# Optimization experiments

Hardware: AMD Instinct MI355X
Metric: run time of the kernel (lower is better)

Reference implementation:

```python
import jax, jax.numpy as jnp
import numpy as np

D = 512        # model dim
NH = 8         # heads
NL = 4         # layers
MSL = 2048     # max_seq_len for relative positional bias
ITEM_V, CATE_V, SEG_V = 100000, 1000, 2
EPS = 1e-5


def layer_norm(x, w, b):
    mu = jnp.mean(x, axis=-1, keepdims=True)
    var = jnp.mean((x - mu) ** 2, axis=-1, keepdims=True)
    return (x - mu) * jax.lax.rsqrt(var + EPS) * w + b


def setup_inputs() -> dict:
    key = jax.random.key(0)
    ks = jax.random.split(key, 16)
    B, L = 8, 1023
    inp = {
        'historical_item_ids': jax.random.randint(ks[0], (B, L), 0, ITEM_V, dtype=jnp.int32),
        'historical_cate_ids': jax.random.randint(ks[1], (B, L), 0, CATE_V, dtype=jnp.int32),
        'historical_len': jax.random.randint(ks[2], (B,), 0, L, dtype=jnp.int32),
        'target_item_id': jax.random.randint(ks[3], (B,), 0, ITEM_V, dtype=jnp.int32),
        'target_cate_id': jax.random.randint(ks[4], (B,), 0, CATE_V, dtype=jnp.int32),
        # embeddings (init std 0.02 like _init_weights)
        'item_emb': 0.02 * jax.random.normal(ks[5], (ITEM_V, D), jnp.float32),
        'cate_emb': 0.02 * jax.random.normal(ks[6], (CATE_V, D), jnp.float32),
        'seg_emb': 0.02 * jax.random.normal(ks[7], (SEG_V, D), jnp.float32),
        # per-layer stacked params
        'W1': 0.02 * jax.random.normal(ks[8], (NL, D, 4 * D), jnp.float32),
        'b1': jnp.zeros((NL, 4 * D), jnp.float32),
        'W2': 0.02 * jax.random.normal(ks[9], (NL, D, D), jnp.float32),
        'b2': jnp.zeros((NL, D), jnp.float32),
        'ln1_w': jnp.ones((NL, D), jnp.float32), 'ln1_b': jnp.zeros((NL, D), jnp.float32),
        'ln2_w': jnp.ones((NL, D), jnp.float32), 'ln2_b': jnp.zeros((NL, D), jnp.float32),
        'pos_w': 0.02 * jax.random.normal(ks[10], (NL, 2 * MSL - 1), jnp.float32),
        'lnf_w': jnp.ones((D,), jnp.float32), 'lnf_b': jnp.zeros((D,), jnp.float32),
    }
    return inp


def _forward(historical_item_ids, historical_cate_ids, historical_len,
             target_item_id, target_cate_id,
             item_emb, cate_emb, seg_emb, W1, b1, W2, b2,
             ln1_w, ln1_b, ln2_w, ln2_b, pos_w, lnf_w, lnf_b):
    B = historical_item_ids.shape[0]
    ar = jnp.arange(B)
    pad = jnp.zeros((B, 1), historical_item_ids.dtype)
    ids = jnp.concatenate([historical_item_ids, pad], axis=1).at[ar, historical_len].set(target_item_id)
    cids = jnp.concatenate([historical_cate_ids, pad], axis=1).at[ar, historical_len].set(target_cate_id)
    S = ids.shape[1]
    seg = jnp.zeros_like(ids).at[ar, historical_len].set(1)

    h = item_emb[ids] + cate_emb[cids] + seg_emb[seg]  # [B,S,D]

    # relative position bias indices: bias[i,j] = pos_w[MSL-1 + j - i]
    rel_idx = MSL - 1 + jnp.arange(S)[None, :] - jnp.arange(S)[:, None]  # [S,S]
    causal = jnp.tril(jnp.ones((S, S), h.dtype))  # multiplicative mask (mask >= 0)

    for l in range(NL):
        z = jax.nn.silu(h @ W1[l] + b1[l])  # [B,S,4D]
        u, q, k, v = jnp.split(z, 4, axis=-1)
        resh = lambda t: t.reshape(B, S, NH, D // NH).transpose(0, 2, 1, 3)  # [B,H,S,hd]
        u, q, k, v = resh(u), resh(q), resh(k), resh(v)
        bias = pos_w[l][rel_idx]  # [S,S]
        att = jax.nn.silu(jnp.einsum('bhsd,bhtd->bhst', q, k) + bias) * causal
        y = jnp.einsum('bhst,bhtd->bhsd', att, v) * u
        y = y.transpose(0, 2, 1, 3).reshape(B, S, D)
        y = layer_norm(y, ln1_w[l], ln1_b[l])
        y = y @ W2[l] + b2[l]
        h = layer_norm(y + h, ln2_w[l], ln2_b[l])  # dropout p=0 (eval)

    return layer_norm(h, lnf_w, lnf_b)


def reference(historical_item_ids, historical_cate_ids, historical_len,
              target_item_id, target_cate_id,
              item_emb, cate_emb, seg_emb, W1, b1, W2, b2,
              ln1_w, ln1_b, ln2_w, ln2_b, pos_w, lnf_w, lnf_b):
    return _forward(historical_item_ids, historical_cate_ids, historical_len,
                    target_item_id, target_cate_id,
                    item_emb, cate_emb, seg_emb, W1, b1, W2, b2,
                    ln1_w, ln1_b, ln2_w, ln2_b, pos_w, lnf_w, lnf_b)
```

## Files before the change

### kernel.cpp

```cpp
#include <hip/hip_runtime.h>
#include <cstddef>


#define D_MODEL 512
#define S_LEN 1024
#define NHEADS 8

typedef __bf16 bf16x8 __attribute__((ext_vector_type(8)));
typedef float f32x4 __attribute__((ext_vector_type(4)));
typedef unsigned short us4 __attribute__((ext_vector_type(4)));
typedef unsigned short us8 __attribute__((ext_vector_type(8)));

__device__ __forceinline__ float silu_f(float x) {
  return x / (1.f + __expf(-x));
}
__device__ __forceinline__ unsigned short f2bf(float f) {
  unsigned int u = __float_as_uint(f);
  u += 0x7FFF + ((u >> 16) & 1);
  return (unsigned short)(u >> 16);
}
__device__ __forceinline__ float bf2f(unsigned short s) {
  return __uint_as_float(((unsigned int)s) << 16);
}
__device__ __forceinline__ void gll16(const void* g, void* l) {
  __builtin_amdgcn_global_load_lds(
      (const __attribute__((address_space(1))) unsigned int*)g,
      (__attribute__((address_space(3))) unsigned int*)l, 16, 0, 0);
}

__global__ __launch_bounds__(256) void embed_kernel(
    const int* __restrict__ hist_i, const int* __restrict__ hist_c,
    const int* __restrict__ hlen, const int* __restrict__ tgt_i,
    const int* __restrict__ tgt_c, const float* __restrict__ item_emb,
    const float* __restrict__ cate_emb, const float* __restrict__ seg_emb,
    float* __restrict__ h32, unsigned short* __restrict__ hbf) {
  int bs = blockIdx.x;
  int b = bs >> 10, s = bs & 1023;
  int l = hlen[b];
  int id, cid, sg;
  if (s == l)       { id = tgt_i[b]; cid = tgt_c[b]; sg = 1; }
  else if (s < 1023){ id = hist_i[b * 1023 + s]; cid = hist_c[b * 1023 + s]; sg = 0; }
  else              { id = 0; cid = 0; sg = 0; }
  const float* ie = item_emb + (size_t)id * D_MODEL;
  const float* ce = cate_emb + (size_t)cid * D_MODEL;
  const float* se = seg_emb + (size_t)sg * D_MODEL;
  float* hr = h32 + (size_t)bs * D_MODEL;
  unsigned short* hb = hbf + (size_t)bs * D_MODEL;
  for (int d = threadIdx.x; d < D_MODEL; d += 256) {
    float v = ie[d] + ce[d] + se[d];
    hr[d] = v;
    hb[d] = f2bf(v);
  }
}

__global__ __launch_bounds__(256) void transpose_kernel(
    const float* __restrict__ W, unsigned short* __restrict__ Wt,
    int K, int N) {
  const int l = blockIdx.z;
  W += (size_t)l * K * N;
  Wt += (size_t)l * K * N;
  const int n0 = blockIdx.x * 64, k0 = blockIdx.y * 64;
  __shared__ float T[64][65];
  const int tid = threadIdx.x;
  const int rr = tid >> 4, cc = (tid & 15) * 4;
#pragma unroll
  for (int p = 0; p < 4; p++) {
    const int r = rr + p * 16;
    const float4 v = *reinterpret_cast<const float4*>(&W[(size_t)(k0 + r) * N + n0 + cc]);
    T[r][cc] = v.x; T[r][cc + 1] = v.y; T[r][cc + 2] = v.z; T[r][cc + 3] = v.w;
  }
  __syncthreads();
#pragma unroll
  for (int p = 0; p < 4; p++) {
    const int r = rr + p * 16;
    us4 o = { f2bf(T[cc + 0][r]), f2bf(T[cc + 1][r]),
              f2bf(T[cc + 2][r]), f2bf(T[cc + 3][r]) };
    *reinterpret_cast<us4*>(&Wt[(size_t)(n0 + r) * K + k0 + cc]) = o;
  }
}

template <int TM, int TN, int SWZ, int EPI_SILU, typename OutT>
__global__ __launch_bounds__(256) void mfma_gemm(
    const unsigned short* __restrict__ A, const unsigned short* __restrict__ Bt,
    const float* __restrict__ bias, OutT* __restrict__ C,
    int M, int N, int K) {
  constexpr int MI = TM / 32, NI = TN / 32;
  __shared__ unsigned short As[2][TM * 64];
  __shared__ unsigned short Bs[2][TN * 64];
  const int tid = threadIdx.x;
  const int w = tid >> 6, lane = tid & 63, lm = lane & 15, quad = lane >> 4;
  const int wm = w & 1, wn = w >> 1;
  int m0, n0;
  if (SWZ) {
    const int id = blockIdx.x;
    const int xcd = id & 7, j = id >> 3;
    const int mPerX = (M / TM) >> 3;
    m0 = (xcd * mPerX + (j % mPerX)) * TM;
    n0 = (j / mPerX) * TN;
  } else {
    m0 = blockIdx.y * TM;
    n0 = blockIdx.x * TN;
  }

  f32x4 acc[MI][NI] = {};

  auto stage = [&](int buf, int k0) {
#pragma unroll
    for (int p = 0; p < TM / 32; p++) {
      const int g = p * 256 + tid;
      const int r = g >> 3;
      const int lc = (g & 7) ^ (r & 7);
      gll16(A + (size_t)(m0 + r) * K + k0 + lc * 8, &As[buf][g * 8]);
    }
#pragma unroll
    for (int p = 0; p < TN / 32; p++) {
      const int g = p * 256 + tid;
      const int r = g >> 3;
      const int lc = (g & 7) ^ (r & 7);
      gll16(Bt + (size_t)(n0 + r) * K + k0 + lc * 8, &Bs[buf][g * 8]);
    }
  };

  stage(0, 0);
  __syncthreads();
  int cur = 0;

  for (int k0 = 0; k0 < K; k0 += 64) {
    if (k0 + 64 < K) stage(cur ^ 1, k0 + 64);
#pragma unroll
    for (int ki = 0; ki < 2; ki++) {
      bf16x8 af[MI], bfr[NI];
#pragma unroll
      for (int mi = 0; mi < MI; mi++) {
        const int r = wm * (TM / 2) + mi * 16 + lm;
        const int p = (ki * 4 + quad) ^ (lm & 7);
        af[mi] = *reinterpret_cast<const bf16x8*>(&As[cur][r * 64 + p * 8]);
      }
#pragma unroll
      for (int ni = 0; ni < NI; ni++) {
        const int r = wn * (TN / 2) + ni * 16 + lm;
        const int p = (ki * 4 + quad) ^ (lm & 7);
        bfr[ni] = *reinterpret_cast<const bf16x8*>(&Bs[cur][r * 64 + p * 8]);
      }
#pragma unroll
      for (int mi = 0; mi < MI; mi++)
#pragma unroll
        for (int ni = 0; ni < NI; ni++)
          acc[mi][ni] = __builtin_amdgcn_mfma_f32_16x16x32_bf16(
              af[mi], bfr[ni], acc[mi][ni], 0, 0, 0);
    }
    __syncthreads();
    cur ^= 1;
  }

#pragma unroll
  for (int ni = 0; ni < NI; ni++) {
    const int n = n0 + wn * (TN / 2) + ni * 16 + lm;
    const float bv = bias[n];
#pragma unroll
    for (int mi = 0; mi < MI; mi++) {
      const int mbase = m0 + wm * (TM / 2) + mi * 16 + quad * 4;
#pragma unroll
      for (int reg = 0; reg < 4; reg++) {
        float v = acc[mi][ni][reg] + bv;
        if (EPI_SILU) v = silu_f(v);
        if constexpr (sizeof(OutT) == 2)
          C[(size_t)(mbase + reg) * N + n] = f2bf(v);
        else
          C[(size_t)(mbase + reg) * N + n] = v;
      }
    }
  }
}

#define LDR 72
__global__ __launch_bounds__(256) void attn_kernel(
    const unsigned short* __restrict__ z, const float* __restrict__ posw,
    unsigned short* __restrict__ y) {
  const int hh = blockIdx.y, b = blockIdx.z;
  __shared__ alignas(16) unsigned short Ks[2 * 64 * LDR];
  __shared__ alignas(16) unsigned short Vt[2 * 64 * LDR];
  __shared__ alignas(16) unsigned short Ps[64 * LDR];
  __shared__ float bias_s[2][128];
  const unsigned short* zb = z + (size_t)b * S_LEN * 2048;
  const int tid = threadIdx.x;
  const int w = tid >> 6, lane = tid & 63, lm = lane & 15, quad = lane >> 4;

  const int kr0r = tid >> 3, kr0c = (tid & 7) * 8;
  const int kr1r = (256 + tid) >> 3, kr1c = (tid & 7) * 8;
  const int vt = (tid >> 4) * 4, vd = (tid & 15) * 4;
  const int vtb = vt >> 3, vti = vt & 7;

#pragma unroll
  for (int phase = 0; phase < 2; phase++) {
    const int qt = phase == 0 ? (int)blockIdx.x : 15 - (int)blockIdx.x;
    const int s0 = qt * 64;
    const int srow = s0 + w * 16 + lm;

    const bf16x8 qb0 = *reinterpret_cast<const bf16x8*>(
        zb + (size_t)srow * 2048 + 512 + hh * 64 + quad * 8);
    const bf16x8 qb1 = *reinterpret_cast<const bf16x8*>(
        zb + (size_t)srow * 2048 + 512 + hh * 64 + 32 + quad * 8);

    f32x4 O[4] = {};

    us8 kr0, kr1;
    us4 vr0, vr1, vr2, vr3;
    float br = 0.f;

    auto load_stage = [&](int kt) {
      const int t0 = kt * 64;
      kr0 = *reinterpret_cast<const us8*>(
          zb + (size_t)(t0 + kr0r) * 2048 + 1024 + hh * 64 + kr0c);
      kr1 = *reinterpret_cast<const us8*>(
          zb + (size_t)(t0 + kr1r) * 2048 + 1024 + hh * 64 + kr1c);
      vr0 = *reinterpret_cast<const us4*>(
          zb + (size_t)(t0 + vt + 0) * 2048 + 1536 + hh * 64 + vd);
      vr1 = *reinterpret_cast<const us4*>(
          zb + (size_t)(t0 + vt + 1) * 2048 + 1536 + hh * 64 + vd);
      vr2 = *reinterpret_cast<const us4*>(
          zb + (size_t)(t0 + vt + 2) * 2048 + 1536 + hh * 64 + vd);
      vr3 = *reinterpret_cast<const us4*>(
          zb + (size_t)(t0 + vt + 3) * 2048 + 1536 + hh * 64 + vd);
      if (tid < 128) br = posw[2047 + t0 - s0 - 63 + tid];
    };

    auto write_stage = [&](int cur) {
      unsigned short* KsC = Ks + cur * (64 * LDR);
      unsigned short* VtC = Vt + cur * (64 * LDR);
      *reinterpret_cast<us8*>(&KsC[kr0r * LDR + kr0c]) = kr0;
      *reinterpret_cast<us8*>(&KsC[kr1r * LDR + kr1c]) = kr1;
      unsigned short c[4][4];
      c[0][0] = vr0.x; c[0][1] = vr0.y; c[0][2] = vr0.z; c[0][3] = vr0.w;
      c[1][0] = vr1.x; c[1][1] = vr1.y; c[1][2] = vr1.z; c[1][3] = vr1.w;
      c[2][0] = vr2.x; c[2][1] = vr2.y; c[2][2] = vr2.z; c[2][3] = vr2.w;
      c[3][0] = vr3.x; c[3][1] = vr3.y; c[3][2] = vr3.z; c[3][3] = vr3.w;
#pragma unroll
      for (int j = 0; j < 4; j++) {
        const int dd = vd + j;
        us4 o = { c[0][j], c[1][j], c[2][j], c[3][j] };
        *reinterpret_cast<us4*>(&VtC[dd * LDR + ((vtb ^ (dd & 7)) << 3) + vti]) = o;
      }
      if (tid < 128) bias_s[cur][tid] = br;
    };

    load_stage(0);
    __syncthreads();

    for (int kt = 0; kt <= qt; kt++) {
      const int cur = kt & 1;
      write_stage(cur);
      __syncthreads();
      if (kt < qt) load_stage(kt + 1);

      const unsigned short* KsC = Ks + cur * (64 * LDR);
      const unsigned short* VtC = Vt + cur * (64 * LDR);
      const int t0 = kt * 64;

#pragma unroll
      for (int tt = 0; tt < 4; tt++) {
        const bf16x8 ka0 = *reinterpret_cast<const bf16x8*>(
            &KsC[(tt * 16 + lm) * LDR + quad * 8]);
        const bf16x8 ka1 = *reinterpret_cast<const bf16x8*>(
            &KsC[(tt * 16 + lm) * LDR + 32 + quad * 8]);
        f32x4 st = {};
        __builtin_amdgcn_s_setprio(1);
        st = __builtin_amdgcn_mfma_f32_16x16x32_bf16(ka0, qb0, st, 0, 0, 0);
        st = __builtin_amdgcn_mfma_f32_16x16x32_bf16(ka1, qb1, st, 0, 0, 0);
        __builtin_amdgcn_s_setprio(0);
        const int bbase = 63 + tt * 16 + quad * 4 - w * 16 - lm;
        const int tq = t0 + tt * 16 + quad * 4;
        us4 pv;
        unsigned short* pp = (unsigned short*)&pv;
#pragma unroll
        for (int i = 0; i < 4; i++) {
          const float x = st[i] + bias_s[cur][bbase + i];
          const float val = (tq + i <= srow) ? silu_f(x) : 0.f;
          pp[i] = f2bf(val);
        }
        *reinterpret_cast<us4*>(&Ps[(w * 16 + lm) * LDR + tt * 16 + quad * 4]) = pv;
      }

      const bf16x8 pa0 = *reinterpret_cast<const bf16x8*>(
          &Ps[(w * 16 + lm) * LDR + quad * 8]);
      const bf16x8 pa1 = *reinterpret_cast<const bf16x8*>(
          &Ps[(w * 16 + lm) * LDR + 32 + quad * 8]);
#pragma unroll
      for (int ct = 0; ct < 4; ct++) {
        const int d = ct * 16 + lm;
        const bf16x8 vb0 = *reinterpret_cast<const bf16x8*>(
            &VtC[d * LDR + ((quad ^ (d & 7)) << 3)]);
        const bf16x8 vb1 = *reinterpret_cast<const bf16x8*>(
            &VtC[d * LDR + (((4 + quad) ^ (d & 7)) << 3)]);
        __builtin_amdgcn_s_setprio(1);
        O[ct] = __builtin_amdgcn_mfma_f32_16x16x32_bf16(pa0, vb0, O[ct], 0, 0, 0);
        O[ct] = __builtin_amdgcn_mfma_f32_16x16x32_bf16(pa1, vb1, O[ct], 0, 0, 0);
        __builtin_amdgcn_s_setprio(0);
      }
    }

    {
      const int sbase = s0 + w * 16 + quad * 4;
#pragma unroll
      for (int ct = 0; ct < 4; ct++) {
        const int d = ct * 16 + lm;
#pragma unroll
        for (int i = 0; i < 4; i++) {
          const int sg = sbase + i;
          const float u = bf2f(zb[(size_t)sg * 2048 + hh * 64 + d]);
          y[((size_t)(b * S_LEN + sg)) * D_MODEL + hh * 64 + d] = f2bf(O[ct][i] * u);
        }
      }
    }
  }
}

template <typename XT>
__global__ __launch_bounds__(256) void ln_kernel(
    const XT* __restrict__ x, const float* __restrict__ res,
    const float* __restrict__ w, const float* __restrict__ bb,
    float* __restrict__ o32, unsigned short* __restrict__ obf) {
  const int wv = threadIdx.x >> 6, lane = threadIdx.x & 63;
  const size_t row = blockIdx.x * 4 + wv;
  const int c0 = lane * 8;
  float v[8];
  if constexpr (sizeof(XT) == 2) {
    const us8 u = *reinterpret_cast<const us8*>(&x[row * D_MODEL + c0]);
#pragma unroll
    for (int i = 0; i < 8; i++) v[i] = bf2f(u[i]);
  } else {
    const float4 a = *reinterpret_cast<const float4*>(&x[row * D_MODEL + c0]);
    const float4 c = *reinterpret_cast<const float4*>(&x[row * D_MODEL + c0 + 4]);
    v[0] = a.x; v[1] = a.y; v[2] = a.z; v[3] = a.w;
    v[4] = c.x; v[5] = c.y; v[6] = c.z; v[7] = c.w;
  }
  if (res) {
    const float4 r0 = *reinterpret_cast<const float4*>(&res[row * D_MODEL + c0]);
    const float4 r1 = *reinterpret_cast<const float4*>(&res[row * D_MODEL + c0 + 4]);
    v[0] += r0.x; v[1] += r0.y; v[2] += r0.z; v[3] += r0.w;
    v[4] += r1.x; v[5] += r1.y; v[6] += r1.z; v[7] += r1.w;
  }
  float s = 0.f, ss = 0.f;
#pragma unroll
  for (int i = 0; i < 8; i++) { s += v[i]; ss += v[i] * v[i]; }
#pragma unroll
  for (int off = 32; off; off >>= 1) {
    s += __shfl_down(s, off, 64);
    ss += __shfl_down(ss, off, 64);
  }
  s = __shfl(s, 0, 64);
  ss = __shfl(ss, 0, 64);
  const float mu = s * (1.f / D_MODEL);
  const float rstd = rsqrtf(ss * (1.f / D_MODEL) - mu * mu + 1e-5f);
  const float4 w0 = *reinterpret_cast<const float4*>(&w[c0]);
  const float4 w1 = *reinterpret_cast<const float4*>(&w[c0 + 4]);
  const float4 b0 = *reinterpret_cast<const float4*>(&bb[c0]);
  const float4 b1 = *reinterpret_cast<const float4*>(&bb[c0 + 4]);
  float r[8];
  r[0] = (v[0] - mu) * rstd * w0.x + b0.x;
  r[1] = (v[1] - mu) * rstd * w0.y + b0.y;
  r[2] = (v[2] - mu) * rstd * w0.z + b0.z;
  r[3] = (v[3] - mu) * rstd * w0.w + b0.w;
  r[4] = (v[4] - mu) * rstd * w1.x + b1.x;
  r[5] = (v[5] - mu) * rstd * w1.y + b1.y;
  r[6] = (v[6] - mu) * rstd * w1.z + b1.z;
  r[7] = (v[7] - mu) * rstd * w1.w + b1.w;
  if (o32) {
    *reinterpret_cast<float4*>(&o32[row * D_MODEL + c0]) = make_float4(r[0], r[1], r[2], r[3]);
    *reinterpret_cast<float4*>(&o32[row * D_MODEL + c0 + 4]) = make_float4(r[4], r[5], r[6], r[7]);
  }
  if (obf) {
    us8 q = { f2bf(r[0]), f2bf(r[1]), f2bf(r[2]), f2bf(r[3]),
              f2bf(r[4]), f2bf(r[5]), f2bf(r[6]), f2bf(r[7]) };
    *reinterpret_cast<us8*>(&obf[row * D_MODEL + c0]) = q;
  }
}

extern "C" void kernel_launch(void* const* d_in, const int* in_sizes, int n_in,
                              void* d_out, int out_size, void* d_ws, size_t ws_size,
                              hipStream_t stream) {
  const int* hist_i = (const int*)d_in[0];
  const int* hist_c = (const int*)d_in[1];
  const int* hlen   = (const int*)d_in[2];
  const int* tgt_i  = (const int*)d_in[3];
  const int* tgt_c  = (const int*)d_in[4];
  const float* item_emb = (const float*)d_in[5];
  const float* cate_emb = (const float*)d_in[6];
  const float* seg_emb  = (const float*)d_in[7];
  const float* W1   = (const float*)d_in[8];
  const float* b1   = (const float*)d_in[9];
  const float* W2   = (const float*)d_in[10];
  const float* b2   = (const float*)d_in[11];
  const float* ln1w = (const float*)d_in[12];
  const float* ln1b = (const float*)d_in[13];
  const float* ln2w = (const float*)d_in[14];
  const float* ln2b = (const float*)d_in[15];
  const float* posw = (const float*)d_in[16];
  const float* lnfw = (const float*)d_in[17];
  const float* lnfb = (const float*)d_in[18];
  float* out = (float*)d_out;

  char* ws = (char*)d_ws;
  float*          h32 = (float*)(ws);
  unsigned short* hbf = (unsigned short*)(ws + (16u << 20));
  unsigned short* zbf = (unsigned short*)(ws + (24u << 20));
  unsigned short* ybf = (unsigned short*)(ws + (56u << 20));
  unsigned short* yab = (unsigned short*)(ws + (64u << 20));
  unsigned short* tbf = yab;
  unsigned short* W1t = (unsigned short*)(ws + (80u << 20));
  unsigned short* W2t = (unsigned short*)(ws + (88u << 20));

  const int ROWS = 8 * S_LEN;

  transpose_kernel<<<dim3(2048 / 64, 512 / 64, 4), 256, 0, stream>>>(W1, W1t, 512, 2048);
  transpose_kernel<<<dim3(512 / 64, 512 / 64, 4), 256, 0, stream>>>(W2, W2t, 512, 512);
  embed_kernel<<<ROWS, 256, 0, stream>>>(hist_i, hist_c, hlen, tgt_i, tgt_c,
                                         item_emb, cate_emb, seg_emb, h32, hbf);
  for (int l = 0; l < 4; l++) {
    mfma_gemm<128, 128, 1, 1, unsigned short><<<1024, 256, 0, stream>>>(
        hbf, W1t + (size_t)l * 2048 * 512, b1 + (size_t)l * 2048, zbf, ROWS, 2048, 512);
    attn_kernel<<<dim3(8, NHEADS, 8), 256, 0, stream>>>(
        zbf, posw + (size_t)l * 4095, yab);
    ln_kernel<unsigned short><<<ROWS / 4, 256, 0, stream>>>(
        yab, nullptr, ln1w + l * 512, ln1b + l * 512, nullptr, ybf);
    mfma_gemm<64, 128, 0, 0, unsigned short><<<dim3(512 / 128, ROWS / 64), 256, 0, stream>>>(
        ybf, W2t + (size_t)l * 512 * 512, b2 + (size_t)l * 512, tbf, ROWS, 512, 512);
    ln_kernel<unsigned short><<<ROWS / 4, 256, 0, stream>>>(
        tbf, h32, ln2w + l * 512, ln2b + l * 512, h32, hbf);
  }
  ln_kernel<float><<<ROWS / 4, 256, 0, stream>>>(h32, nullptr, lnfw, lnfb, out, nullptr);
}
```

Measured before the change: 746.7 us.

## Triple-buffer GEMM loads with vmcnt waits and enlarge W1 GEMM tile

```diff
diff --git a/kernel.cpp b/kernel.cpp
--- a/kernel.cpp
+++ b/kernel.cpp
@@ -79,17 +79,20 @@
   }
 }
 
-template <int TM, int TN, int SWZ, int EPI_SILU, typename OutT>
-__global__ __launch_bounds__(256) void mfma_gemm(
+template <int TM, int TN, int WR, int WC, int SWZ, int EPI_SILU, typename OutT>
+__global__ __launch_bounds__(WR * WC * 64) void mfma_gemm(
     const unsigned short* __restrict__ A, const unsigned short* __restrict__ Bt,
     const float* __restrict__ bias, OutT* __restrict__ C,
     int M, int N, int K) {
-  constexpr int MI = TM / 32, NI = TN / 32;
-  __shared__ unsigned short As[2][TM * 64];
-  __shared__ unsigned short Bs[2][TN * 64];
+  constexpr int NT = WR * WC * 64;
+  constexpr int WM = TM / WR, WN = TN / WC;
+  constexpr int MI = WM / 16, NI = WN / 16;
+  static_assert((TM + TN) * 8 / NT == 6, "vmcnt literal assumes 6 loads/stage");
+  __shared__ unsigned short As[3][TM * 64];
+  __shared__ unsigned short Bs[3][TN * 64];
   const int tid = threadIdx.x;
   const int w = tid >> 6, lane = tid & 63, lm = lane & 15, quad = lane >> 4;
-  const int wm = w & 1, wn = w >> 1;
+  const int wm = w % WR, wn = w / WR;
   int m0, n0;
   if (SWZ) {
     const int id = blockIdx.x;
@@ -106,15 +109,15 @@
 
   auto stage = [&](int buf, int k0) {
 #pragma unroll
-    for (int p = 0; p < TM / 32; p++) {
-      const int g = p * 256 + tid;
+    for (int p = 0; p < TM * 8 / NT; p++) {
+      const int g = p * NT + tid;
       const int r = g >> 3;
       const int lc = (g & 7) ^ (r & 7);
       gll16(A + (size_t)(m0 + r) * K + k0 + lc * 8, &As[buf][g * 8]);
     }
 #pragma unroll
-    for (int p = 0; p < TN / 32; p++) {
-      const int g = p * 256 + tid;
+    for (int p = 0; p < TN * 8 / NT; p++) {
+      const int g = p * NT + tid;
       const int r = g >> 3;
       const int lc = (g & 7) ^ (r & 7);
       gll16(Bt + (size_t)(n0 + r) * K + k0 + lc * 8, &Bs[buf][g * 8]);
@@ -122,44 +125,53 @@
   };
 
   stage(0, 0);
-  __syncthreads();
-  int cur = 0;
+  if (64 < K) stage(1, 64);
+  int cur = 0, nxt = 2;
 
   for (int k0 = 0; k0 < K; k0 += 64) {
-    if (k0 + 64 < K) stage(cur ^ 1, k0 + 64);
+    if (k0 + 64 < K)
+      asm volatile("s_waitcnt vmcnt(6)" ::: "memory");
+    else
+      asm volatile("s_waitcnt vmcnt(0)" ::: "memory");
+    __builtin_amdgcn_s_barrier();
+    __builtin_amdgcn_sched_barrier(0);
+    if (k0 + 128 < K) stage(nxt, k0 + 128);
+
 #pragma unroll
     for (int ki = 0; ki < 2; ki++) {
       bf16x8 af[MI], bfr[NI];
 #pragma unroll
       for (int mi = 0; mi < MI; mi++) {
-        const int r = wm * (TM / 2) + mi * 16 + lm;
+        const int r = wm * WM + mi * 16 + lm;
         const int p = (ki * 4 + quad) ^ (lm & 7);
         af[mi] = *reinterpret_cast<const bf16x8*>(&As[cur][r * 64 + p * 8]);
       }
 #pragma unroll
       for (int ni = 0; ni < NI; ni++) {
-        const int r = wn * (TN / 2) + ni * 16 + lm;
+        const int r = wn * WN + ni * 16 + lm;
         const int p = (ki * 4 + quad) ^ (lm & 7);
         bfr[ni] = *reinterpret_cast<const bf16x8*>(&Bs[cur][r * 64 + p * 8]);
       }
+      __builtin_amdgcn_s_setprio(1);
 #pragma unroll
       for (int mi = 0; mi < MI; mi++)
 #pragma unroll
         for (int ni = 0; ni < NI; ni++)
           acc[mi][ni] = __builtin_amdgcn_mfma_f32_16x16x32_bf16(
               af[mi], bfr[ni], acc[mi][ni], 0, 0, 0);
-    }
-    __syncthreads();
-    cur ^= 1;
+      __builtin_amdgcn_s_setprio(0);
+    }
+    cur = (cur == 2) ? 0 : cur + 1;
+    nxt = (nxt == 2) ? 0 : nxt + 1;
   }
 
 #pragma unroll
   for (int ni = 0; ni < NI; ni++) {
-    const int n = n0 + wn * (TN / 2) + ni * 16 + lm;
+    const int n = n0 + wn * WN + ni * 16 + lm;
     const float bv = bias[n];
 #pragma unroll
     for (int mi = 0; mi < MI; mi++) {
-      const int mbase = m0 + wm * (TM / 2) + mi * 16 + quad * 4;
+      const int mbase = m0 + wm * WM + mi * 16 + quad * 4;
 #pragma unroll
       for (int reg = 0; reg < 4; reg++) {
         float v = acc[mi][ni][reg] + bv;
@@ -417,13 +429,13 @@
   embed_kernel<<<ROWS, 256, 0, stream>>>(hist_i, hist_c, hlen, tgt_i, tgt_c,
                                          item_emb, cate_emb, seg_emb, h32, hbf);
   for (int l = 0; l < 4; l++) {
-    mfma_gemm<128, 128, 1, 1, unsigned short><<<1024, 256, 0, stream>>>(
+    mfma_gemm<256, 128, 4, 2, 1, 1, unsigned short><<<512, 512, 0, stream>>>(
         hbf, W1t + (size_t)l * 2048 * 512, b1 + (size_t)l * 2048, zbf, ROWS, 2048, 512);
     attn_kernel<<<dim3(8, NHEADS, 8), 256, 0, stream>>>(
         zbf, posw + (size_t)l * 4095, yab);
     ln_kernel<unsigned short><<<ROWS / 4, 256, 0, stream>>>(
         yab, nullptr, ln1w + l * 512, ln1b + l * 512, nullptr, ybf);
-    mfma_gemm<64, 128, 0, 0, unsigned short><<<dim3(512 / 128, ROWS / 64), 256, 0, stream>>>(
+    mfma_gemm<64, 128, 2, 2, 0, 0, unsigned short><<<dim3(512 / 128, ROWS / 64), 256, 0, stream>>>(
         ybf, W2t + (size_t)l * 512 * 512, b2 + (size_t)l * 512, tbf, ROWS, 512, 512);
     ln_kernel<unsigned short><<<ROWS / 4, 256, 0, stream>>>(
         tbf, h32, ln2w + l * 512, ln2b + l * 512, h32, hbf);
```

Result: slower. 762.3 us (+2.1%).
